# Kernel optimization log

Hardware: AMD Instinct MI355X
Metric: run time of the kernel (lower is better)

Reference implementation:

```python
import jax, jax.numpy as jnp
import numpy as np

FACTOR = 3
N_HEADS = 8

def _layer_norm(x, g, b, eps=1e-5):
    m = x.mean(-1, keepdims=True)
    v = ((x - m) ** 2).mean(-1, keepdims=True)
    return (x - m) / jnp.sqrt(v + eps) * g + b

def _circ_conv1d(x, w):
    # x: [B, L, Cin], w: [Cout, Cin, 3]; circular padding of 1 (torch padding_mode='circular')
    xp = jnp.pad(x, ((0, 0), (1, 1), (0, 0)), mode='wrap').transpose(0, 2, 1)
    return jax.lax.conv_general_dilated(xp, w, (1,), 'VALID',
                                        dimension_numbers=('NCW', 'OIW', 'NCW'))  # [B, Cout, L]

def _prob_attention(q, k, v, key):
    # q, k, v: [B, H, L, D]; mask_flag=False path of Informer ProbAttention
    B, H, L, D = q.shape
    u = min(FACTOR * int(np.ceil(np.log(L))), L)  # U_part == u for self-attention
    idx = jax.random.randint(key, (L, u), 0, L)   # sampled key indices shared over B, H
    k_samp = k[:, :, idx, :]                       # [B, H, L, u, D]
    qk_samp = jnp.einsum('bhld,bhlud->bhlu', q, k_samp)
    M = qk_samp.max(-1) - qk_samp.sum(-1) / L      # sparsity measurement
    _, m_top = jax.lax.top_k(M, u)                 # [B, H, u] top-u query indices
    q_red = jnp.take_along_axis(q, m_top[..., None], axis=2)   # [B, H, u, D]
    scores = jnp.einsum('bhud,bhld->bhul', q_red, k) * (1.0 / np.sqrt(D))
    attn = jax.nn.softmax(scores, axis=-1)
    upd = jnp.einsum('bhul,bhld->bhud', attn, v)
    ctx = jnp.broadcast_to(v.mean(axis=2, keepdims=True), (B, H, L, D))  # lazy-query context = mean(V)
    bi = jnp.arange(B)[:, None, None]
    hi = jnp.arange(H)[None, :, None]
    ctx = ctx.at[bi, hi, m_top].set(upd)
    return ctx.transpose(0, 2, 1, 3)               # [B, L, H, D]

def _distil(x, w, b, g, beta):
    # ConvLayer: circular conv k=3 -> BatchNorm1d (eval, running stats 0/1) -> ELU -> MaxPool1d(3, 2, pad=1)
    y = _circ_conv1d(x, w) + b[None, :, None]
    y = y / np.sqrt(1.0 + 1e-5) * g[None, :, None] + beta[None, :, None]
    y = jax.nn.elu(y)
    y = jax.lax.reduce_window(y, -jnp.inf, jax.lax.max,
                              (1, 1, 3), (1, 1, 2), ((0, 0), (0, 0), (1, 1)))
    return y.transpose(0, 2, 1)

def _forward(x_enc, emb_w, wq, bq, wk, bk, wv, bv, wo, bo, c1w, c1b, c2w, c2b,
             ln1g, ln1b, ln2g, ln2b, dcw, dcb, bng, bnb, lnfg, lnfb):
    H = N_HEADS
    x = _circ_conv1d(x_enc, emb_w).transpose(0, 2, 1)  # token embedding, [B, L, Dm]
    n_layers = wq.shape[0]
    base = jax.random.key(42)
    for i in range(n_layers):
        B, L, Dm = x.shape
        q = (x @ wq[i].T + bq[i]).reshape(B, L, H, -1).transpose(0, 2, 1, 3)
        k = (x @ wk[i].T + bk[i]).reshape(B, L, H, -1).transpose(0, 2, 1, 3)
        v = (x @ wv[i].T + bv[i]).reshape(B, L, H, -1).transpose(0, 2, 1, 3)
        a = _prob_attention(q, k, v, jax.random.fold_in(base, i)).reshape(B, L, Dm)
        x = x + (a @ wo[i].T + bo[i])
        x = _layer_norm(x, ln1g[i], ln1b[i])
        y = jax.nn.gelu(x @ c1w[i].T + c1b[i], approximate=False)
        y = y @ c2w[i].T + c2b[i]
        x = _layer_norm(x + y, ln2g[i], ln2b[i])
        if i < n_layers - 1:
            x = _distil(x, dcw[i], dcb[i], bng[i], bnb[i])
    x = _layer_norm(x, lnfg, lnfb)
    return x.mean(axis=1)  # [B, Dm]

def setup_inputs() -> dict:
    key = jax.random.key(0)
    ks = jax.random.split(key, 32)
    B, L, C, Dm, Dff, NL = 32, 2048, 7, 512, 512, 3
    s = 0.05
    rn = lambda k, shape: jax.random.normal(k, shape, dtype=jnp.float32) * s
    return {
        'x_enc': jax.random.normal(ks[0], (B, L, C), dtype=jnp.float32),
        'emb_w': rn(ks[1], (Dm, C, 3)),
        'wq': rn(ks[2], (NL, Dm, Dm)), 'bq': rn(ks[3], (NL, Dm)),
        'wk': rn(ks[4], (NL, Dm, Dm)), 'bk': rn(ks[5], (NL, Dm)),
        'wv': rn(ks[6], (NL, Dm, Dm)), 'bv': rn(ks[7], (NL, Dm)),
        'wo': rn(ks[8], (NL, Dm, Dm)), 'bo': rn(ks[9], (NL, Dm)),
        'c1w': rn(ks[10], (NL, Dff, Dm)), 'c1b': rn(ks[11], (NL, Dff)),
        'c2w': rn(ks[12], (NL, Dm, Dff)), 'c2b': rn(ks[13], (NL, Dm)),
        'ln1g': jnp.ones((NL, Dm), jnp.float32), 'ln1b': jnp.zeros((NL, Dm), jnp.float32),
        'ln2g': jnp.ones((NL, Dm), jnp.float32), 'ln2b': jnp.zeros((NL, Dm), jnp.float32),
        'dcw': rn(ks[14], (NL - 1, Dm, Dm, 3)), 'dcb': rn(ks[15], (NL - 1, Dm)),
        'bng': jnp.ones((NL - 1, Dm), jnp.float32), 'bnb': jnp.zeros((NL - 1, Dm), jnp.float32),
        'lnfg': jnp.ones((Dm,), jnp.float32), 'lnfb': jnp.zeros((Dm,), jnp.float32),
    }

def reference(x_enc, emb_w, wq, bq, wk, bk, wv, bv, wo, bo, c1w, c1b, c2w, c2b,
              ln1g, ln1b, ln2g, ln2b, dcw, dcb, bng, bnb, lnfg, lnfb):
    return _forward(x_enc, emb_w, wq, bq, wk, bk, wv, bv, wo, bo, c1w, c1b, c2w, c2b,
                    ln1g, ln1b, ln2g, ln2b, dcw, dcb, bng, bnb, lnfg, lnfb)
```

## Files before the change

kernel.cpp:

```cpp
#include <hip/hip_runtime.h>
#include <stdint.h>

#define DM 512
#define DH 64

typedef __bf16 bf16x8 __attribute__((ext_vector_type(8)));
typedef float f32x4 __attribute__((ext_vector_type(4)));

__device__ __forceinline__ float bf2f(unsigned short h) {
  union { unsigned int u; float f; } c; c.u = ((unsigned int)h) << 16; return c.f;
}
__device__ __forceinline__ unsigned short f2bf(float f) {
  union { float f; unsigned int u; } c; c.f = f;
  unsigned int u = c.u;
  return (unsigned short)((u + 0x7FFFu + ((u >> 16) & 1u)) >> 16);
}
__device__ __forceinline__ void unpack8(uint4 v, float* f) {
  f[0] = bf2f((unsigned short)(v.x & 0xffff)); f[1] = bf2f((unsigned short)(v.x >> 16));
  f[2] = bf2f((unsigned short)(v.y & 0xffff)); f[3] = bf2f((unsigned short)(v.y >> 16));
  f[4] = bf2f((unsigned short)(v.z & 0xffff)); f[5] = bf2f((unsigned short)(v.z >> 16));
  f[6] = bf2f((unsigned short)(v.w & 0xffff)); f[7] = bf2f((unsigned short)(v.w >> 16));
}
__device__ __forceinline__ float dot8(uint4 kv, const float* qf) {
  float s;
  s  = bf2f((unsigned short)(kv.x & 0xffff)) * qf[0];
  s += bf2f((unsigned short)(kv.x >> 16))    * qf[1];
  s += bf2f((unsigned short)(kv.y & 0xffff)) * qf[2];
  s += bf2f((unsigned short)(kv.y >> 16))    * qf[3];
  s += bf2f((unsigned short)(kv.z & 0xffff)) * qf[4];
  s += bf2f((unsigned short)(kv.z >> 16))    * qf[5];
  s += bf2f((unsigned short)(kv.w & 0xffff)) * qf[6];
  s += bf2f((unsigned short)(kv.w >> 16))    * qf[7];
  return s;
}

__host__ __device__ inline void tf2x32(uint32_t k0, uint32_t k1, uint32_t x0, uint32_t x1,
                                       uint32_t* o0, uint32_t* o1) {
  uint32_t ks2 = k0 ^ k1 ^ 0x1BD11BDAu;
#define TFR(r) { x0 += x1; x1 = (x1 << r) | (x1 >> (32 - r)); x1 ^= x0; }
  x0 += k0; x1 += k1;
  TFR(13) TFR(15) TFR(26) TFR(6)
  x0 += k1; x1 += ks2 + 1u;
  TFR(17) TFR(29) TFR(16) TFR(24)
  x0 += ks2; x1 += k0 + 2u;
  TFR(13) TFR(15) TFR(26) TFR(6)
  x0 += k0; x1 += k1 + 3u;
  TFR(17) TFR(29) TFR(16) TFR(24)
  x0 += k1; x1 += ks2 + 4u;
  TFR(13) TFR(15) TFR(26) TFR(6)
  *o0 = x0 + ks2; *o1 = x1 + k0 + 5u;
#undef TFR
}

__global__ void idx_kernel(int* __restrict__ idx, int nhalf, unsigned int k0, unsigned int k1, int mask) {
  int m = blockIdx.x * 256 + threadIdx.x;
  if (m >= nhalf) return;
  uint32_t o0, o1;
  tf2x32(k0, k1, (uint32_t)m, (uint32_t)(m + nhalf), &o0, &o1);
  idx[m] = (int)(o0 & (uint32_t)mask);
  idx[m + nhalf] = (int)(o1 & (uint32_t)mask);
}

__device__ __forceinline__ void async_copy16(void* lds, const void* g) {
  __builtin_amdgcn_global_load_lds((const __attribute__((address_space(1))) unsigned int*)g,
                                   (__attribute__((address_space(3))) unsigned int*)lds,
                                   16, 0, 0);
}

template<int EPI, int CIRC>
__global__ __launch_bounds__(256) void gemm_bt(
    const unsigned short* __restrict__ A, const unsigned short* __restrict__ Bw,
    const float* __restrict__ bias, float* __restrict__ Cf, unsigned short* __restrict__ Cb,
    int M, int N, int K, int L, int Lsh, size_t qkvs, int NBN, int xswz)
{
  __shared__ unsigned short sA[128 * 64];
  __shared__ unsigned short sB[128 * 64];
  const int tid = threadIdx.x;
  const int wave = tid >> 6, lane = tid & 63;

  int blk = blockIdx.x;
  if (xswz) { int cpx = (int)gridDim.x >> 3; blk = (blk & 7) * cpx + (blk >> 3); }
  const int bn = blk % NBN, bm = blk / NBN;

  const int wm = (wave >> 1) << 6, wn = (wave & 1) << 6;

  const int srow = (wave << 5) + (lane >> 3);
  const int kb = (((lane & 7) ^ ((lane >> 3) & 7)) << 3);

  const unsigned short* gA = nullptr;
  int bA = 0, lI = 0;
  if constexpr (CIRC) {
    int r = bm * 128 + srow;
    bA = r >> Lsh; lI = r & (L - 1);
  } else {
    gA = A + (size_t)(bm * 128 + srow) * K + kb;
  }
  const unsigned short* gB = Bw + (size_t)(bn * 128 + srow) * K + kb;

  f32x4 acc[4][4] = {};

  for (int k0 = 0; k0 < K; k0 += 64) {
#pragma unroll
    for (int q = 0; q < 4; q++) {
      unsigned short* ldsA = &sA[((wave << 5) + (q << 3)) << 6];
      unsigned short* ldsB = &sB[((wave << 5) + (q << 3)) << 6];
      if constexpr (CIRC) {
        int t = k0 >> 9;
        int kk = (k0 & 511) + kb;
        int sl = (lI + (q << 3) - 1 + t + L) & (L - 1);
        int bq = (bm * 128 + srow + (q << 3)) >> Lsh;
        async_copy16(ldsA, A + (((size_t)(bq * L + sl)) << 9) + kk);
      } else {
        async_copy16(ldsA, gA + (size_t)(q << 3) * K + k0);
      }
      async_copy16(ldsB, gB + (size_t)(q << 3) * K + k0);
    }
    __syncthreads();
#pragma unroll
    for (int kk = 0; kk < 2; kk++) {
      bf16x8 af[4], bfr[4];
#pragma unroll
      for (int i = 0; i < 4; i++) {
        int row = wm + (i << 4) + (lane & 15);
        int slot = ((kk << 2) + (lane >> 4)) ^ (lane & 7);
        af[i] = *(const bf16x8*)&sA[(row << 6) + (slot << 3)];
      }
#pragma unroll
      for (int j = 0; j < 4; j++) {
        int row = wn + (j << 4) + (lane & 15);
        int slot = ((kk << 2) + (lane >> 4)) ^ (lane & 7);
        bfr[j] = *(const bf16x8*)&sB[(row << 6) + (slot << 3)];
      }
#pragma unroll
      for (int i = 0; i < 4; i++)
#pragma unroll
        for (int j = 0; j < 4; j++)
          acc[i][j] = __builtin_amdgcn_mfma_f32_16x16x32_bf16(af[i], bfr[j], acc[i][j], 0, 0, 0);
    }
    __syncthreads();
  }

  const int cr = (lane >> 4) << 2;
  const int cc = lane & 15;
#pragma unroll
  for (int j = 0; j < 4; j++) {
    const int col = (bn << 7) + wn + (j << 4) + cc;
    const float bvv = bias[col];
#pragma unroll
    for (int i = 0; i < 4; i++) {
      const size_t row = (size_t)(bm << 7) + wm + (i << 4) + cr;
#pragma unroll
      for (int r = 0; r < 4; r++) {
        float v = acc[i][j][r] + bvv;
        if constexpr (EPI == 0) {
          Cf[(row + r) * (size_t)N + col] = v;
        } else if constexpr (EPI == 1) {
          Cb[(row + r) * (size_t)N + col] = f2bf(v);
        } else if constexpr (EPI == 2) {
          float ge = 0.5f * v * (1.0f + erff(v * 0.70710678118654752f));
          Cb[(row + r) * (size_t)N + col] = f2bf(ge);
        } else {
          Cb[(size_t)(col >> 9) * qkvs + ((row + r) << 9) + (col & 511)] = f2bf(v);
        }
      }
    }
  }
}

__global__ __launch_bounds__(256) void embed_kernel(const float* __restrict__ xe,
    const float* __restrict__ w, unsigned short* __restrict__ xb)
{
  int blk = blockIdx.x;
  int b = blk >> 6, lg = blk & 63;
  int l0 = lg << 5;
  int tid = threadIdx.x;
  __shared__ float xwin[34 * 7];
  for (int i = tid; i < 34 * 7; i += 256) {
    int r = i / 7, c = i - r * 7;
    int sl = (l0 - 1 + r) & 2047;
    xwin[i] = xe[((size_t)(b * 2048 + sl)) * 7 + c];
  }
  __syncthreads();
  float wr0[21], wr1[21];
  const float* w0 = w + tid * 21;
  const float* w1 = w + (tid + 256) * 21;
#pragma unroll
  for (int k = 0; k < 21; k++) { wr0[k] = w0[k]; wr1[k] = w1[k]; }
#pragma unroll 1
  for (int ll = 0; ll < 32; ll++) {
    float a0 = 0.0f, a1 = 0.0f;
#pragma unroll
    for (int c = 0; c < 7; c++)
#pragma unroll
      for (int t = 0; t < 3; t++) {
        float xv = xwin[(ll + t) * 7 + c];
        a0 += xv * wr0[c * 3 + t];
        a1 += xv * wr1[c * 3 + t];
      }
    size_t o = ((size_t)(b * 2048 + l0 + ll)) << 9;
    xb[o + tid] = f2bf(a0);
    xb[o + 256 + tid] = f2bf(a1);
  }
}

template<int U>
__global__ __launch_bounds__(256) void msamp_kernel(
    const unsigned short* __restrict__ qb, const unsigned short* __restrict__ kbuf,
    const int* __restrict__ idx, float* __restrict__ Mv, int L, int nlc, float invL,
    int xcdgrp)
{
  const int RB = 16;
  int blk = blockIdx.x;
  int b, lc;
  if (xcdgrp) {
    int xcd = blk & 7, slot = blk >> 3;
    int g = slot / nlc; lc = slot - g * nlc;
    b = g * 8 + xcd;
  } else {
    b = blk / nlc; lc = blk - b * nlc;
  }
  int l0 = lc * RB;
  int tid = threadIdx.x;
  int wave = tid >> 6, lane = tid & 63;
  int p = lane & 7, h = lane >> 3;
  __shared__ int iidx[RB * U];
  __shared__ float pM[RB * 8 * 25];

  for (int i = tid; i < RB * U; i += 256) iidx[i] = idx[l0 * U + i];
  __syncthreads();

  const size_t rowbase = ((size_t)(b * L)) << 9;
#pragma unroll
  for (int r = 0; r < RB / 4; r++) {
    int l = wave * (RB / 4) + r;
    uint4 qv = *(const uint4*)(qb + rowbase + (((size_t)(l0 + l)) << 9) + (lane << 3));
    float qf[8]; unpack8(qv, qf);
    int kr[U];
#pragma unroll
    for (int j = 0; j < U; j++) kr[j] = iidx[l * U + j];
#pragma unroll
    for (int j = 0; j < U; j++) {
      uint4 kv = *(const uint4*)(kbuf + rowbase + (((size_t)kr[j]) << 9) + (lane << 3));
      float s = dot8(kv, qf);
      s += __shfl_xor(s, 1);
      s += __shfl_xor(s, 2);
      s += __shfl_xor(s, 4);
      if (p == 0) pM[(l * 8 + h) * 25 + j] = s;
    }
  }
  __syncthreads();

  if (tid < RB * 8) {
    int l = tid >> 3, hh = tid & 7;
    float mx = -3.0e38f, sm = 0.0f;
    const float* pr = &pM[tid * 25];
    for (int j = 0; j < U; j++) { float v = pr[j]; mx = fmaxf(mx, v); sm += v; }
    Mv[((size_t)((b << 3) + hh)) * L + l0 + l] = mx - sm * invL;
  }
}

template<int S>
__global__ __launch_bounds__(256) void topk_kernel(const float* __restrict__ Mv,
    int* __restrict__ mtop, int L, int u)
{
  int bh = blockIdx.x; int tid = threadIdx.x;
  int wave = tid >> 6, lane = tid & 63;
  float lv[S];
#pragma unroll
  for (int s = 0; s < S; s++) lv[s] = Mv[(size_t)bh * L + s * 256 + tid];
  __shared__ float sv[4];
  __shared__ int si[4];
  for (int t = 0; t < u; t++) {
    float bv = lv[0]; int bs = 0;
#pragma unroll
    for (int s = 1; s < S; s++) if (lv[s] > bv) { bv = lv[s]; bs = s; }
    int bi = bs * 256 + tid;
#pragma unroll
    for (int o = 1; o < 64; o <<= 1) {
      float ov = __shfl_xor(bv, o); int oi = __shfl_xor(bi, o);
      if (ov > bv || (ov == bv && oi < bi)) { bv = ov; bi = oi; }
    }
    if (lane == 0) { sv[wave] = bv; si[wave] = bi; }
    __syncthreads();
    float wv = sv[0]; int wi = si[0];
#pragma unroll
    for (int w = 1; w < 4; w++) {
      float ov = sv[w]; int oi = si[w];
      if (ov > wv || (ov == wv && oi < wi)) { wv = ov; wi = oi; }
    }
    if (tid == 0) mtop[bh * u + t] = wi;
#pragma unroll
    for (int s = 0; s < S; s++)
      if (s == (wi >> 8) && (wi & 255) == tid) lv[s] = -3.0e38f;
    __syncthreads();
  }
}

template<int U>
__device__ __forceinline__ void dot_rows(const unsigned short* __restrict__ krow,
                                         const float* __restrict__ qred, float* s)
{
#pragma unroll
  for (int j = 0; j < U; j++) s[j] = 0.0f;
  const uint4* kv4 = (const uint4*)krow;
#pragma unroll
  for (int d8 = 0; d8 < 8; d8++) {
    uint4 kv = kv4[d8];
    float kf[8];
    kf[0] = bf2f((unsigned short)(kv.x & 0xffff)); kf[1] = bf2f((unsigned short)(kv.x >> 16));
    kf[2] = bf2f((unsigned short)(kv.y & 0xffff)); kf[3] = bf2f((unsigned short)(kv.y >> 16));
    kf[4] = bf2f((unsigned short)(kv.z & 0xffff)); kf[5] = bf2f((unsigned short)(kv.z >> 16));
    kf[6] = bf2f((unsigned short)(kv.w & 0xffff)); kf[7] = bf2f((unsigned short)(kv.w >> 16));
#pragma unroll
    for (int j = 0; j < U; j++) {
      const float4 q0 = *(const float4*)&qred[j * 64 + d8 * 8];
      const float4 q1 = *(const float4*)&qred[j * 64 + d8 * 8 + 4];
      s[j] += kf[0] * q0.x + kf[1] * q0.y + kf[2] * q0.z + kf[3] * q0.w
            + kf[4] * q1.x + kf[5] * q1.y + kf[6] * q1.z + kf[7] * q1.w;
    }
  }
}

template<int U>
__global__ __launch_bounds__(256) void attn_part(
    const unsigned short* __restrict__ qb, const unsigned short* __restrict__ kbuf,
    const unsigned short* __restrict__ vbuf, const int* __restrict__ mtop,
    float* __restrict__ pupd, float* __restrict__ pden, float* __restrict__ pvs,
    int L, int S)
{
  int blk = blockIdx.x;
  int bh = blk / S, split = blk - bh * S;
  int b = bh >> 3, h = bh & 7;
  int tid = threadIdx.x;
  __shared__ float qred[U * 64];
  __shared__ float pA[U * 4 * 66];
  __shared__ float pB[U * 256];
  __shared__ float pC[256];
  __shared__ float dnred[4 * U];

  for (int i = tid; i < U * 64; i += 256) {
    int j = i >> 6, d = i & 63;
    int row = mtop[bh * U + j];
    qred[i] = bf2f(qb[(((size_t)(b * L + row)) << 9) + h * 64 + d]) * 0.125f;
  }
  __syncthreads();

  int l = (split << 8) + tid;
  {
    float s[U];
    dot_rows<U>(kbuf + (((size_t)(b * L + l)) << 9) + h * 64, qred, s);
    int g0 = tid >> 6, d0 = tid & 63;
#pragma unroll
    for (int j = 0; j < U; j++) pA[(j * 4 + g0) * 66 + d0] = expf(s[j]);
  }
  __syncthreads();

  int g = tid >> 6, d = tid & 63;
  const unsigned short* vcol = vbuf + (((size_t)(b * L)) << 9) + h * 64 + d;
  float lupd[U], ldn[U]; float lvs = 0.0f;
#pragma unroll
  for (int j = 0; j < U; j++) { lupd[j] = 0.0f; ldn[j] = 0.0f; }
#pragma unroll 1
  for (int li = 0; li < 64; li++) {
    int ll = (split << 8) + (g << 6) + li;
    float vd = bf2f(vcol[(size_t)ll << 9]);
    lvs += vd;
#pragma unroll
    for (int j = 0; j < U; j++) {
      float pv = pA[(j * 4 + g) * 66 + li];
      ldn[j] += pv; lupd[j] += pv * vd;
    }
  }
  if (d == 0) {
#pragma unroll
    for (int j = 0; j < U; j++) dnred[g * U + j] = ldn[j];
  }
#pragma unroll
  for (int j = 0; j < U; j++) pB[(g * U + j) * 64 + d] = lupd[j];
  pC[tid] = lvs;
  __syncthreads();

  size_t base = (size_t)bh * S + split;
  for (int i = tid; i < U * 64; i += 256) {
    int j = i >> 6, dd = i & 63;
    pupd[base * (U * 64) + i] = pB[j * 64 + dd] + pB[(U + j) * 64 + dd]
                              + pB[(2 * U + j) * 64 + dd] + pB[(3 * U + j) * 64 + dd];
  }
  if (tid < U)
    pden[base * U + tid] = dnred[tid] + dnred[U + tid] + dnred[2 * U + tid] + dnred[3 * U + tid];
  if (tid < 64)
    pvs[base * 64 + tid] = pC[tid] + pC[64 + tid] + pC[128 + tid] + pC[192 + tid];
}

template<int U>
__global__ __launch_bounds__(256) void attn_comb(
    const int* __restrict__ mtop, const float* __restrict__ pupd,
    const float* __restrict__ pden, const float* __restrict__ pvs,
    unsigned short* __restrict__ ab, int L, int S)
{
  int bh = blockIdx.x; int b = bh >> 3, h = bh & 7;
  int tid = threadIdx.x;
  __shared__ float updf[U * 64];
  __shared__ float den[U];
  __shared__ float vm[64];
  for (int i = tid; i < U * 64; i += 256) {
    float s = 0.0f;
    for (int sp = 0; sp < S; sp++) s += pupd[((size_t)bh * S + sp) * (U * 64) + i];
    updf[i] = s;
  }
  if (tid < U) {
    float s = 0.0f;
    for (int sp = 0; sp < S; sp++) s += pden[((size_t)bh * S + sp) * U + tid];
    den[tid] = s;
  }
  if (tid < 64) {
    float s = 0.0f;
    for (int sp = 0; sp < S; sp++) s += pvs[((size_t)bh * S + sp) * 64 + tid];
    vm[tid] = s / (float)L;
  }
  __syncthreads();
  int g = tid >> 6, d = tid & 63;
  unsigned short vmb = f2bf(vm[d]);
  for (int l = g; l < L; l += 4)
    ab[(((size_t)(b * L + l)) << 9) + h * 64 + d] = vmb;
  __syncthreads();
  for (int i = tid; i < U * 64; i += 256) {
    int j = i >> 6, dd = i & 63;
    int row = mtop[bh * U + j];
    ab[(((size_t)(b * L + row)) << 9) + h * 64 + dd] = f2bf(updf[i] / den[j]);
  }
}

__global__ __launch_bounds__(256) void ln_kernel(const float* __restrict__ xin,
    const unsigned short* __restrict__ residb, const float* __restrict__ g,
    const float* __restrict__ beta, unsigned short* __restrict__ xbout,
    float* __restrict__ xfout)
{
  size_t base = (size_t)blockIdx.x * 512; int tid = threadIdx.x;
  float v0 = 0.0f, v1 = 0.0f;
  if (xin)    { v0 += xin[base + tid]; v1 += xin[base + 256 + tid]; }
  if (residb) { v0 += bf2f(residb[base + tid]); v1 += bf2f(residb[base + 256 + tid]); }
  __shared__ float red[256];
  __shared__ float smean, srstd;
  red[tid] = v0 + v1; __syncthreads();
  for (int s = 128; s > 0; s >>= 1) { if (tid < s) red[tid] += red[tid + s]; __syncthreads(); }
  if (tid == 0) smean = red[0] * (1.0f / 512.0f);
  __syncthreads();
  float m = smean;
  float d0 = v0 - m, d1 = v1 - m;
  red[tid] = d0 * d0 + d1 * d1; __syncthreads();
  for (int s = 128; s > 0; s >>= 1) { if (tid < s) red[tid] += red[tid + s]; __syncthreads(); }
  if (tid == 0) srstd = rsqrtf(red[0] * (1.0f / 512.0f) + 1e-5f);
  __syncthreads();
  float rs = srstd;
  float o0 = d0 * rs * g[tid] + beta[tid];
  float o1 = d1 * rs * g[tid + 256] + beta[tid + 256];
  if (xbout) { xbout[base + tid] = f2bf(o0); xbout[base + 256 + tid] = f2bf(o1); }
  if (xfout) { xfout[base + tid] = o0; xfout[base + 256 + tid] = o1; }
}

__global__ void pool_kernel(const float* __restrict__ z, const float* __restrict__ g,
    const float* __restrict__ beta, unsigned short* __restrict__ xbout, int L, int count)
{
  int i = blockIdx.x * 256 + threadIdx.x;
  if (i >= count) return;
  int o = i & 511; int r1 = i >> 9;
  int Lh = L >> 1;
  int l2 = r1 % Lh; int b = r1 / Lh;
  const float invs = 0.99999500003749969f;
  float gg = g[o] * invs, bb = beta[o];
  float m = -3.0e38f;
#pragma unroll
  for (int w = -1; w <= 1; w++) {
    int l = 2 * l2 + w;
    if (l >= 0 && l < L) {
      float y = z[(size_t)(b * L + l) * DM + o] * gg + bb;
      y = (y > 0.0f) ? y : expm1f(y);
      m = fmaxf(m, y);
    }
  }
  xbout[(size_t)(b * Lh + l2) * DM + o] = f2bf(m);
}

__global__ void cvt_kernel(const float* __restrict__ in, unsigned short* __restrict__ out, int n) {
  int i = blockIdx.x * 256 + threadIdx.x;
  if (i < n) out[i] = f2bf(in[i]);
}

__global__ void cvt_qkv(const float* __restrict__ src, unsigned short* __restrict__ dst, int matoff) {
  int i = blockIdx.x * 256 + threadIdx.x;
  if (i >= 786432) return;
  int layer = i >> 18; int rem = i & 262143;
  dst[(size_t)layer * 786432 + matoff + rem] = f2bf(src[i]);
}

__global__ void catbias(const float* __restrict__ bq, const float* __restrict__ bk,
                        const float* __restrict__ bv, float* __restrict__ dst) {
  int i = blockIdx.x * 256 + threadIdx.x;
  if (i >= 3 * 1536) return;
  int layer = i / 1536, c = i - layer * 1536;
  float v = (c < 512) ? bq[layer * 512 + c]
          : (c < 1024) ? bk[layer * 512 + c - 512]
          : bv[layer * 512 + c - 1024];
  dst[i] = v;
}

__global__ void repack_dcw(const float* __restrict__ dcw, unsigned short* __restrict__ wt, int n) {
  int i = blockIdx.x * 256 + threadIdx.x;
  if (i >= n) return;
  int t = i % 3; int rest = i / 3; int c = rest % 512; int lo = rest / 512;
  wt[(size_t)lo * 1536 + t * 512 + c] = f2bf(dcw[i]);
}

__global__ void mean_part(const float* __restrict__ xin, float* __restrict__ part, int nblkPerB) {
  int blk = blockIdx.x;
  int b = blk / nblkPerB, pc = blk - b * nblkPerB;
  int tid = threadIdx.x;
  float s0 = 0.0f, s1 = 0.0f;
  int l0 = pc * 32;
  for (int r = 0; r < 32; r++) {
    size_t base = ((size_t)(b * 512 + l0 + r)) << 9;
    s0 += xin[base + tid];
    s1 += xin[base + 256 + tid];
  }
  part[((size_t)blk << 9) + tid] = s0;
  part[((size_t)blk << 9) + 256 + tid] = s1;
}
__global__ void mean_fin(const float* __restrict__ part, float* __restrict__ out,
                         int nblkPerB, int nb) {
  int i = blockIdx.x * 256 + threadIdx.x;
  if (i >= nb * 512) return;
  int b = i >> 9, d = i & 511;
  float s = 0.0f;
  for (int c = 0; c < nblkPerB; c++) s += part[((size_t)(b * nblkPerB + c) << 9) + d];
  out[i] = s * (1.0f / 512.0f);
}

extern "C" void kernel_launch(void* const* d_in, const int* in_sizes, int n_in,
                              void* d_out, int out_size, void* d_ws, size_t ws_size,
                              hipStream_t stream)
{
  (void)in_sizes; (void)n_in; (void)out_size;
  const float* x_enc = (const float*)d_in[0];
  const float* emb_w = (const float*)d_in[1];
  const float* wq   = (const float*)d_in[2];
  const float* bq   = (const float*)d_in[3];
  const float* wk   = (const float*)d_in[4];
  const float* bk   = (const float*)d_in[5];
  const float* wv   = (const float*)d_in[6];
  const float* bvv  = (const float*)d_in[7];
  const float* wo   = (const float*)d_in[8];
  const float* bo   = (const float*)d_in[9];
  const float* c1w  = (const float*)d_in[10];
  const float* c1b  = (const float*)d_in[11];
  const float* c2w  = (const float*)d_in[12];
  const float* c2b  = (const float*)d_in[13];
  const float* ln1g = (const float*)d_in[14];
  const float* ln1b = (const float*)d_in[15];
  const float* ln2g = (const float*)d_in[16];
  const float* ln2b = (const float*)d_in[17];
  const float* dcw  = (const float*)d_in[18];
  const float* dcb  = (const float*)d_in[19];
  const float* bng  = (const float*)d_in[20];
  const float* bnb  = (const float*)d_in[21];
  const float* lnfg = (const float*)d_in[22];
  const float* lnfb = (const float*)d_in[23];

  int nb = 32;
  while (nb > 1 && (16777216ull + (size_t)nb * 8804352ull) > ws_size) nb >>= 1;

  char* ws = (char*)d_ws;
  size_t off = 0;
  unsigned short* WQKV = (unsigned short*)(ws + off); off += 4718592ull;
  unsigned short* WOB  = (unsigned short*)(ws + off); off += 1572864ull;
  unsigned short* C1WB = (unsigned short*)(ws + off); off += 1572864ull;
  unsigned short* C2WB = (unsigned short*)(ws + off); off += 1572864ull;
  unsigned short* WTB  = (unsigned short*)(ws + off); off += 3145728ull;
  float* BQKVB         = (float*)(ws + off);          off += 18432ull;
  float* MP            = (float*)(ws + off);          off += 2097152ull;
  int* IDXP            = (int*)(ws + off);            off += 589824ull;
  int* MTOPP           = (int*)(ws + off);            off += 24576ull;

  size_t cb = 16777216ull;
  unsigned short* Xbf = (unsigned short*)(ws + cb);
  char* R             = ws + cb + (size_t)nb * 2097152ull;
  unsigned short* DQ  = (unsigned short*)R;
  unsigned short* DK  = (unsigned short*)(R + (size_t)nb * 2097152ull);
  unsigned short* DV  = (unsigned short*)(R + (size_t)nb * 4194304ull);
  float* TMP          = (float*)R;
  unsigned short* AB  = DV;
  float* PUPD         = (float*)(ws + cb + (size_t)nb * 8388608ull);
  float* PDEN         = (float*)((char*)PUPD + (size_t)nb * 393216ull);
  float* PVS          = (float*)((char*)PDEN + (size_t)nb * 6144ull);
  const size_t qkvs   = (size_t)nb * 1048576ull;

  {
    int nw = 3 * 512 * 512;
    int blocks = (nw + 255) / 256;
    cvt_qkv<<<blocks, 256, 0, stream>>>(wq, WQKV, 0);
    cvt_qkv<<<blocks, 256, 0, stream>>>(wk, WQKV, 262144);
    cvt_qkv<<<blocks, 256, 0, stream>>>(wv, WQKV, 524288);
    catbias<<<18, 256, 0, stream>>>(bq, bk, bvv, BQKVB);
    cvt_kernel<<<blocks, 256, 0, stream>>>(wo,  WOB,  nw);
    cvt_kernel<<<blocks, 256, 0, stream>>>(c1w, C1WB, nw);
    cvt_kernel<<<blocks, 256, 0, stream>>>(c2w, C2WB, nw);
    int nd = 2 * 512 * 512 * 3;
    repack_dcw<<<(nd + 255) / 256, 256, 0, stream>>>(dcw, WTB, nd);
  }

  for (int layer = 0; layer < 3; layer++) {
    int Ll = (layer == 0) ? 2048 : (layer == 1 ? 1024 : 512);
    int ul = (layer == 0) ? 24 : 21;
    uint32_t f0, f1, a0, b0k, a1, b1k;
    tf2x32(0u, 42u, 0u, (uint32_t)layer, &f0, &f1);
    tf2x32(f0, f1, 0u, 2u, &a0, &b0k);
    tf2x32(f0, f1, 1u, 3u, &a1, &b1k);
    (void)a0; (void)a1;
    int nhalf = Ll * ul / 2;
    idx_kernel<<<(nhalf + 255) / 256, 256, 0, stream>>>(IDXP + layer * 49152, nhalf, b0k, b1k, Ll - 1);
  }

  for (int b0 = 0; b0 < 32; b0 += nb) {
    embed_kernel<<<nb * 64, 256, 0, stream>>>(x_enc + (size_t)b0 * 2048 * 7, emb_w, Xbf);

    int L = 2048, Lsh = 11;
    for (int layer = 0; layer < 3; layer++) {
      const int M_ = nb * L;
      const int u = (layer == 0) ? 24 : 21;
      const int S = L >> 8;
      const int nbm = M_ / 128;
      const int ng  = 4 * nbm;
      const int ngq = 12 * nbm;
      const int xsg  = (ng  % 8 == 0) ? 1 : 0;
      const int xsgq = (ngq % 8 == 0) ? 1 : 0;
      const int xg = (nb % 8 == 0) ? 1 : 0;

      gemm_bt<3,0><<<ngq, 256, 0, stream>>>(Xbf, WQKV + (size_t)layer * 786432, BQKVB + layer * 1536, nullptr, DQ, M_, 1536, 512, 0, 0, qkvs, 12, xsgq);

      if (u == 24) msamp_kernel<24><<<nb * (L / 16), 256, 0, stream>>>(DQ, DK, IDXP + layer * 49152, MP, L, L / 16, 1.0f / (float)L, xg);
      else         msamp_kernel<21><<<nb * (L / 16), 256, 0, stream>>>(DQ, DK, IDXP + layer * 49152, MP, L, L / 16, 1.0f / (float)L, xg);

      if (L == 2048)      topk_kernel<8><<<nb * 8, 256, 0, stream>>>(MP, MTOPP, L, u);
      else if (L == 1024) topk_kernel<4><<<nb * 8, 256, 0, stream>>>(MP, MTOPP, L, u);
      else                topk_kernel<2><<<nb * 8, 256, 0, stream>>>(MP, MTOPP, L, u);

      if (u == 24) {
        attn_part<24><<<nb * 8 * S, 256, 0, stream>>>(DQ, DK, DV, MTOPP, PUPD, PDEN, PVS, L, S);
        attn_comb<24><<<nb * 8, 256, 0, stream>>>(MTOPP, PUPD, PDEN, PVS, AB, L, S);
      } else {
        attn_part<21><<<nb * 8 * S, 256, 0, stream>>>(DQ, DK, DV, MTOPP, PUPD, PDEN, PVS, L, S);
        attn_comb<21><<<nb * 8, 256, 0, stream>>>(MTOPP, PUPD, PDEN, PVS, AB, L, S);
      }

      gemm_bt<0,0><<<ng, 256, 0, stream>>>(AB, WOB + (size_t)layer * 262144, bo + layer * 512, TMP, nullptr, M_, 512, 512, 0, 0, 0, 4, xsg);
      ln_kernel<<<M_, 256, 0, stream>>>(TMP, Xbf, ln1g + layer * 512, ln1b + layer * 512, Xbf, nullptr);
      gemm_bt<2,0><<<ng, 256, 0, stream>>>(Xbf, C1WB + (size_t)layer * 262144, c1b + layer * 512, nullptr, AB, M_, 512, 512, 0, 0, 0, 4, xsg);
      gemm_bt<0,0><<<ng, 256, 0, stream>>>(AB, C2WB + (size_t)layer * 262144, c2b + layer * 512, TMP, nullptr, M_, 512, 512, 0, 0, 0, 4, xsg);
      ln_kernel<<<M_, 256, 0, stream>>>(TMP, Xbf, ln2g + layer * 512, ln2b + layer * 512, Xbf, nullptr);

      if (layer < 2) {
        gemm_bt<0,1><<<ng, 256, 0, stream>>>(Xbf, WTB + (size_t)layer * 786432, dcb + layer * 512, TMP, nullptr, M_, 512, 1536, L, Lsh, 0, 4, xsg);
        pool_kernel<<<nb * L, 256, 0, stream>>>(TMP, bng + layer * 512, bnb + layer * 512, Xbf, L, nb * (L / 2) * 512);
        L >>= 1; Lsh -= 1;
      }
    }

    ln_kernel<<<nb * 512, 256, 0, stream>>>(nullptr, Xbf, lnfg, lnfb, nullptr, TMP);
    mean_part<<<nb * 16, 256, 0, stream>>>(TMP, MP, 16);
    mean_fin<<<(nb * 512 + 255) / 256, 256, 0, stream>>>(MP, (float*)d_out + (size_t)b0 * 512, 16, nb);
  }
}
```

Measured before the change: 2.235 ms.

## Stage GEMM epilogue through LDS for vectorized bf16 stores; make intermediates bf16

The GEMM epilogue now writes each 16-row slice of the accumulator tile into shared memory as bf16, then stores it to global memory as coalesced 16-byte vectors instead of scattered 2- or 4-byte writes. The fp32 intermediate buffers (output projection, FFN second GEMM, distil conv output) become bf16, and the layernorm and pool kernels read bf16 instead of fp32. This halves the intermediate traffic and improves store coalescing. In exchange it adds extra barriers in the epilogue and rounds the pre-layernorm and pre-pool sums to bf16, which loses precision.

```diff
diff --git a/kernel.cpp b/kernel.cpp
--- a/kernel.cpp
+++ b/kernel.cpp
@@ -70,7 +70,7 @@
 template<int EPI, int CIRC>
 __global__ __launch_bounds__(256) void gemm_bt(
     const unsigned short* __restrict__ A, const unsigned short* __restrict__ Bw,
-    const float* __restrict__ bias, float* __restrict__ Cf, unsigned short* __restrict__ Cb,
+    const float* __restrict__ bias, unsigned short* __restrict__ Cb,
     int M, int N, int K, int L, int Lsh, size_t qkvs, int NBN, int xswz)
 {
   __shared__ unsigned short sA[128 * 64];
@@ -88,10 +88,10 @@
   const int kb = (((lane & 7) ^ ((lane >> 3) & 7)) << 3);
 
   const unsigned short* gA = nullptr;
-  int bA = 0, lI = 0;
+  int lI = 0;
   if constexpr (CIRC) {
     int r = bm * 128 + srow;
-    bA = r >> Lsh; lI = r & (L - 1);
+    lI = r & (L - 1);
   } else {
     gA = A + (size_t)(bm * 128 + srow) * K + kb;
   }
@@ -140,28 +140,38 @@
     __syncthreads();
   }
 
+  unsigned short* sOut = sA;
   const int cr = (lane >> 4) << 2;
   const int cc = lane & 15;
-#pragma unroll
-  for (int j = 0; j < 4; j++) {
-    const int col = (bn << 7) + wn + (j << 4) + cc;
-    const float bvv = bias[col];
-#pragma unroll
-    for (int i = 0; i < 4; i++) {
-      const size_t row = (size_t)(bm << 7) + wm + (i << 4) + cr;
+  const int lrb = ((wave >> 1) << 4) + cr;
+#pragma unroll 1
+  for (int i = 0; i < 4; i++) {
+    if (i) __syncthreads();
+#pragma unroll
+    for (int j = 0; j < 4; j++) {
+      const int col = wn + (j << 4) + cc;
+      const float bvv = bias[(bn << 7) + col];
 #pragma unroll
       for (int r = 0; r < 4; r++) {
         float v = acc[i][j][r] + bvv;
-        if constexpr (EPI == 0) {
-          Cf[(row + r) * (size_t)N + col] = v;
-        } else if constexpr (EPI == 1) {
-          Cb[(row + r) * (size_t)N + col] = f2bf(v);
-        } else if constexpr (EPI == 2) {
-          float ge = 0.5f * v * (1.0f + erff(v * 0.70710678118654752f));
-          Cb[(row + r) * (size_t)N + col] = f2bf(ge);
-        } else {
-          Cb[(size_t)(col >> 9) * qkvs + ((row + r) << 9) + (col & 511)] = f2bf(v);
+        if constexpr (EPI == 2) {
+          v = 0.5f * v * (1.0f + erff(v * 0.70710678118654752f));
         }
+        sOut[(lrb + r) * 136 + col] = f2bf(v);
+      }
+    }
+    __syncthreads();
+    int lr = tid >> 3, ch0 = tid & 7;
+    int grow = (bm << 7) + ((lr >> 4) << 6) + (i << 4) + (lr & 15);
+#pragma unroll
+    for (int cpart = 0; cpart < 2; cpart++) {
+      int ch = ch0 + (cpart << 3);
+      uint4 val = *(const uint4*)&sOut[lr * 136 + (ch << 3)];
+      if constexpr (EPI == 3) {
+        int gcol = (bn << 7) + (ch << 3);
+        *(uint4*)&Cb[(size_t)(gcol >> 9) * qkvs + ((size_t)grow << 9) + (gcol & 511)] = val;
+      } else {
+        *(uint4*)&Cb[(size_t)grow * N + (bn << 7) + (ch << 3)] = val;
       }
     }
   }
@@ -431,14 +441,14 @@
   }
 }
 
-__global__ __launch_bounds__(256) void ln_kernel(const float* __restrict__ xin,
+__global__ __launch_bounds__(256) void ln_kernel(const unsigned short* __restrict__ xinb,
     const unsigned short* __restrict__ residb, const float* __restrict__ g,
     const float* __restrict__ beta, unsigned short* __restrict__ xbout,
     float* __restrict__ xfout)
 {
   size_t base = (size_t)blockIdx.x * 512; int tid = threadIdx.x;
   float v0 = 0.0f, v1 = 0.0f;
-  if (xin)    { v0 += xin[base + tid]; v1 += xin[base + 256 + tid]; }
+  if (xinb)   { v0 += bf2f(xinb[base + tid]); v1 += bf2f(xinb[base + 256 + tid]); }
   if (residb) { v0 += bf2f(residb[base + tid]); v1 += bf2f(residb[base + 256 + tid]); }
   __shared__ float red[256];
   __shared__ float smean, srstd;
@@ -459,7 +469,7 @@
   if (xfout) { xfout[base + tid] = o0; xfout[base + 256 + tid] = o1; }
 }
 
-__global__ void pool_kernel(const float* __restrict__ z, const float* __restrict__ g,
+__global__ void pool_kernel(const unsigned short* __restrict__ z, const float* __restrict__ g,
     const float* __restrict__ beta, unsigned short* __restrict__ xbout, int L, int count)
 {
   int i = blockIdx.x * 256 + threadIdx.x;
@@ -474,7 +484,7 @@
   for (int w = -1; w <= 1; w++) {
     int l = 2 * l2 + w;
     if (l >= 0 && l < L) {
-      float y = z[(size_t)(b * L + l) * DM + o] * gg + bb;
+      float y = bf2f(z[(size_t)(b * L + l) * DM + o]) * gg + bb;
       y = (y > 0.0f) ? y : expm1f(y);
       m = fmaxf(m, y);
     }
@@ -582,17 +592,18 @@
   int* MTOPP           = (int*)(ws + off);            off += 24576ull;
 
   size_t cb = 16777216ull;
-  unsigned short* Xbf = (unsigned short*)(ws + cb);
-  char* R             = ws + cb + (size_t)nb * 2097152ull;
-  unsigned short* DQ  = (unsigned short*)R;
-  unsigned short* DK  = (unsigned short*)(R + (size_t)nb * 2097152ull);
-  unsigned short* DV  = (unsigned short*)(R + (size_t)nb * 4194304ull);
-  float* TMP          = (float*)R;
-  unsigned short* AB  = DV;
-  float* PUPD         = (float*)(ws + cb + (size_t)nb * 8388608ull);
-  float* PDEN         = (float*)((char*)PUPD + (size_t)nb * 393216ull);
-  float* PVS          = (float*)((char*)PDEN + (size_t)nb * 6144ull);
-  const size_t qkvs   = (size_t)nb * 1048576ull;
+  unsigned short* Xbf  = (unsigned short*)(ws + cb);
+  char* R              = ws + cb + (size_t)nb * 2097152ull;
+  unsigned short* DQ   = (unsigned short*)R;
+  unsigned short* DK   = (unsigned short*)(R + (size_t)nb * 2097152ull);
+  unsigned short* DV   = (unsigned short*)(R + (size_t)nb * 4194304ull);
+  unsigned short* TMPB = DQ;
+  float* TMPF          = (float*)DK;
+  unsigned short* AB   = DV;
+  float* PUPD          = (float*)(ws + cb + (size_t)nb * 8388608ull);
+  float* PDEN          = (float*)((char*)PUPD + (size_t)nb * 393216ull);
+  float* PVS           = (float*)((char*)PDEN + (size_t)nb * 6144ull);
+  const size_t qkvs    = (size_t)nb * 1048576ull;
 
   {
     int nw = 3 * 512 * 512;
@@ -635,7 +646,7 @@
       const int xsgq = (ngq % 8 == 0) ? 1 : 0;
       const int xg = (nb % 8 == 0) ? 1 : 0;
 
-      gemm_bt<3,0><<<ngq, 256, 0, stream>>>(Xbf, WQKV + (size_t)layer * 786432, BQKVB + layer * 1536, nullptr, DQ, M_, 1536, 512, 0, 0, qkvs, 12, xsgq);
+      gemm_bt<3,0><<<ngq, 256, 0, stream>>>(Xbf, WQKV + (size_t)layer * 786432, BQKVB + layer * 1536, DQ, M_, 1536, 512, 0, 0, qkvs, 12, xsgq);
 
       if (u == 24) msamp_kernel<24><<<nb * (L / 16), 256, 0, stream>>>(DQ, DK, IDXP + layer * 49152, MP, L, L / 16, 1.0f / (float)L, xg);
       else         msamp_kernel<21><<<nb * (L / 16), 256, 0, stream>>>(DQ, DK, IDXP + layer * 49152, MP, L, L / 16, 1.0f / (float)L, xg);
@@ -652,21 +663,21 @@
         attn_comb<21><<<nb * 8, 256, 0, stream>>>(MTOPP, PUPD, PDEN, PVS, AB, L, S);
       }
 
-      gemm_bt<0,0><<<ng, 256, 0, stream>>>(AB, WOB + (size_t)layer * 262144, bo + layer * 512, TMP, nullptr, M_, 512, 512, 0, 0, 0, 4, xsg);
-      ln_kernel<<<M_, 256, 0, stream>>>(TMP, Xbf, ln1g + layer * 512, ln1b + layer * 512, Xbf, nullptr);
-      gemm_bt<2,0><<<ng, 256, 0, stream>>>(Xbf, C1WB + (size_t)layer * 262144, c1b + layer * 512, nullptr, AB, M_, 512, 512, 0, 0, 0, 4, xsg);
-      gemm_bt<0,0><<<ng, 256, 0, stream>>>(AB, C2WB + (size_t)layer * 262144, c2b + layer * 512, TMP, nullptr, M_, 512, 512, 0, 0, 0, 4, xsg);
-      ln_kernel<<<M_, 256, 0, stream>>>(TMP, Xbf, ln2g + layer * 512, ln2b + layer * 512, Xbf, nullptr);
+      gemm_bt<1,0><<<ng, 256, 0, stream>>>(AB, WOB + (size_t)layer * 262144, bo + layer * 512, TMPB, M_, 512, 512, 0, 0, 0, 4, xsg);
+      ln_kernel<<<M_, 256, 0, stream>>>(TMPB, Xbf, ln1g + layer * 512, ln1b + layer * 512, Xbf, nullptr);
+      gemm_bt<2,0><<<ng, 256, 0, stream>>>(Xbf, C1WB + (size_t)layer * 262144, c1b + layer * 512, AB, M_, 512, 512, 0, 0, 0, 4, xsg);
+      gemm_bt<1,0><<<ng, 256, 0, stream>>>(AB, C2WB + (size_t)layer * 262144, c2b + layer * 512, TMPB, M_, 512, 512, 0, 0, 0, 4, xsg);
+      ln_kernel<<<M_, 256, 0, stream>>>(TMPB, Xbf, ln2g + layer * 512, ln2b + layer * 512, Xbf, nullptr);
 
       if (layer < 2) {
-        gemm_bt<0,1><<<ng, 256, 0, stream>>>(Xbf, WTB + (size_t)layer * 786432, dcb + layer * 512, TMP, nullptr, M_, 512, 1536, L, Lsh, 0, 4, xsg);
-        pool_kernel<<<nb * L, 256, 0, stream>>>(TMP, bng + layer * 512, bnb + layer * 512, Xbf, L, nb * (L / 2) * 512);
+        gemm_bt<1,1><<<ng, 256, 0, stream>>>(Xbf, WTB + (size_t)layer * 786432, dcb + layer * 512, TMPB, M_, 512, 1536, L, Lsh, 0, 4, xsg);
+        pool_kernel<<<nb * L, 256, 0, stream>>>(TMPB, bng + layer * 512, bnb + layer * 512, Xbf, L, nb * (L / 2) * 512);
         L >>= 1; Lsh -= 1;
       }
     }
 
-    ln_kernel<<<nb * 512, 256, 0, stream>>>(nullptr, Xbf, lnfg, lnfb, nullptr, TMP);
-    mean_part<<<nb * 16, 256, 0, stream>>>(TMP, MP, 16);
+    ln_kernel<<<nb * 512, 256, 0, stream>>>(nullptr, Xbf, lnfg, lnfb, nullptr, TMPF);
+    mean_part<<<nb * 16, 256, 0, stream>>>(TMPF, MP, 16);
     mean_fin<<<(nb * 512 + 255) / 256, 256, 0, stream>>>(MP, (float*)d_out + (size_t)b0 * 512, 16, nb);
   }
 }
```

After: 7.270 ms. 225% more time.
